# Kernel tuning notes

Measured on AMD Instinct MI355X. Metric: run time of the kernel, lower is better.

The kernel has to match this reference:

```python
import jax, jax.numpy as jnp
import numpy as np

N, F_IN, H, C, E = 100000, 512, 16, 40, 3200000
EPS = 1e-5


def setup_inputs() -> dict:
    key = jax.random.key(0)
    ks = jax.random.split(key, 8)
    x = jax.random.normal(ks[0], (N, F_IN), dtype=jnp.float32)
    edge_index = jax.random.randint(ks[1], (2, E), 0, N, dtype=jnp.int64)
    s1 = 1.0 / np.sqrt(F_IN)
    s2 = 1.0 / np.sqrt(H)
    W1 = jax.random.uniform(ks[2], (F_IN, H), jnp.float32, -s1, s1)
    b1 = jnp.zeros((H,), jnp.float32)
    W2 = jax.random.uniform(ks[3], (H, C), jnp.float32, -s2, s2)
    b2 = jnp.zeros((C,), jnp.float32)
    gamma = jnp.ones((H,), jnp.float32)
    beta = jnp.zeros((H,), jnp.float32)
    return {"x": x, "edge_index": edge_index, "W1": W1, "b1": b1,
            "W2": W2, "b2": b2, "gamma": gamma, "beta": beta}


def gcn_conv(x, edge_index, W, b):
    # PyG GCNConv: linear transform, add self-loops, symmetric normalization,
    # scatter-add aggregation at target nodes (edge_index[1]).
    xw = x @ W  # [N, out]
    loops = jnp.arange(N, dtype=edge_index.dtype)
    row = jnp.concatenate([edge_index[0], loops])  # sources
    col = jnp.concatenate([edge_index[1], loops])  # targets
    deg = jax.ops.segment_sum(jnp.ones_like(col, dtype=xw.dtype), col, num_segments=N)
    dis = jnp.where(deg > 0, jax.lax.rsqrt(deg), 0.0)
    norm = dis[row] * dis[col]  # [E+N]
    msgs = norm[:, None] * xw[row]
    out = jax.ops.segment_sum(msgs, col, num_segments=N)
    return out + b


def batch_norm(x, gamma, beta):
    mean = jnp.mean(x, axis=0)
    var = jnp.var(x, axis=0)
    return (x - mean) * jax.lax.rsqrt(var + EPS) * gamma + beta


def reference(x, edge_index, W1, b1, W2, b2, gamma, beta):
    h = jax.nn.relu(gcn_conv(x, edge_index, W1, b1))
    h = batch_norm(h, gamma, beta)
    # dropout omitted (deterministic reference / eval)
    h = gcn_conv(h, edge_index, W2, b2)
    return jax.nn.log_softmax(h, axis=1)
```

## Files before the change

kernel.cpp:

```cpp
#include <hip/hip_runtime.h>

#define NN 100000
#define FIN 512
#define HD 16
#define CD 40
#define NE 3200000
#define EPSV 1e-5f
#define NBUK 391
#define CAP 9216
#define CH 4096
#define NBLK_CNT ((NE + CH - 1) / CH)
#define NBLK_MM ((NN / 16 + 3) / 4)
#define NSTAT 256

typedef __attribute__((ext_vector_type(8))) short short8;
typedef __attribute__((ext_vector_type(4))) float f32x4;

static __device__ __forceinline__ short f2bf(float f) {
  union { float f; unsigned u; } a; a.f = f;
  unsigned r = a.u + 0x7fffu + ((a.u >> 16) & 1u);
  return (short)(r >> 16);
}
static __device__ __forceinline__ float bf2f(unsigned short u) {
  union { unsigned u; float f; } a; a.u = (unsigned)u << 16; return a.f;
}

__global__ void k_init(int* __restrict__ bkcur, int* __restrict__ gbase) {
  int i = threadIdx.x;
  if (i < NBUK) bkcur[i] = 0;
  if (i == 0) *gbase = 0;
}

__global__ void __launch_bounds__(256) k_fat(const int* __restrict__ ei,
                                             int* __restrict__ bkcur,
                                             unsigned* __restrict__ part,
                                             const float* __restrict__ x,
                                             const float* __restrict__ W1,
                                             float* __restrict__ xw) {
  __shared__ unsigned stg[CH];
  __shared__ unsigned spk[CH];
  __shared__ int hist[NBUK];
  __shared__ int lbase[NBUK + 1];
  __shared__ int gb[NBUK];
  int t = threadIdx.x;
  if (blockIdx.x % 3 == 0) {
    int pb = blockIdx.x / 3;
    int e0 = pb * CH;
    int n = NE - e0; if (n > CH) n = CH;
    for (int i = t; i < NBUK; i += 256) hist[i] = 0;
    for (int i = t; i < n; i += 256) stg[i] = (unsigned)ei[NE + e0 + i];
    __syncthreads();
    for (int i = t; i < n; i += 256) atomicAdd(&hist[stg[i] >> 8], 1);
    __syncthreads();
    if (t < 64) {
      int c0 = t * 7;
      int loc[7]; int s = 0;
#pragma unroll
      for (int k = 0; k < 7; k++) {
        int idx = c0 + k;
        int v = (idx < NBUK) ? hist[idx] : 0;
        loc[k] = s; s += v;
      }
      int inc = s;
#pragma unroll
      for (int m = 1; m < 64; m <<= 1) {
        int u = __shfl_up(inc, m);
        if (t >= m) inc += u;
      }
      int base0 = inc - s;
#pragma unroll
      for (int k = 0; k < 7; k++) {
        int idx = c0 + k;
        if (idx < NBUK) lbase[idx] = base0 + loc[k];
      }
      if (t == 63) lbase[NBUK] = base0 + s;
    }
    __syncthreads();
    for (int i = t; i < NBUK; i += 256) {
      int c = hist[i];
      gb[i] = (c > 0) ? atomicAdd(&bkcur[i], c) : 0;
    }
    __syncthreads();
    for (int i = t; i < NBUK; i += 256) hist[i] = lbase[i];
    __syncthreads();
    for (int i = t; i < n; i += 256) {
      unsigned tg = stg[i];
      int b = tg >> 8;
      int pos = atomicAdd(&hist[b], 1);
      spk[pos] = (unsigned)ei[e0 + i] | ((tg & 255u) << 20);
    }
    __syncthreads();
    for (int b = t; b < NBUK; b += 256) {
      int s0 = lbase[b], s1 = lbase[b + 1];
      for (int j = s0; j < s1; j++) stg[j] = (unsigned)b;
    }
    __syncthreads();
    for (int i = t; i < n; i += 256) {
      int b = (int)stg[i];
      int slot = gb[b] + (i - lbase[b]);
      if (slot < CAP) part[(size_t)b * CAP + slot] = spk[i];
    }
  } else {
    int mb = blockIdx.x - blockIdx.x / 3 - 1;
    int wave = t >> 6;
    int lane = t & 63;
    int tile = mb * 4 + wave;
    int row0 = tile * 16;
    if (row0 >= NN) return;
    int lr = lane & 15;
    int kg = lane >> 4;

    short8 bfrag[16];
#pragma unroll
    for (int s = 0; s < 16; s++) {
      int kbase = s * 32 + kg * 8;
      short8 bf;
#pragma unroll
      for (int i = 0; i < 8; i++) bf[i] = f2bf(W1[(kbase + i) * HD + lr]);
      bfrag[s] = bf;
    }

    f32x4 acc = {0.f, 0.f, 0.f, 0.f};
    const float* xrow = x + (size_t)(row0 + lr) * FIN + kg * 8;
    f32x4 a0[4], a1[4];
#pragma unroll
    for (int p = 0; p < 3; p++) {
      a0[p] = *(const f32x4*)(xrow + p * 32);
      a1[p] = *(const f32x4*)(xrow + p * 32 + 4);
    }
#pragma unroll
    for (int s = 0; s < 16; s++) {
      if (s < 13) {
        a0[(s + 3) & 3] = *(const f32x4*)(xrow + (s + 3) * 32);
        a1[(s + 3) & 3] = *(const f32x4*)(xrow + (s + 3) * 32 + 4);
      }
      f32x4 u0 = a0[s & 3], u1 = a1[s & 3];
      short8 af;
      af[0] = f2bf(u0.x); af[1] = f2bf(u0.y); af[2] = f2bf(u0.z); af[3] = f2bf(u0.w);
      af[4] = f2bf(u1.x); af[5] = f2bf(u1.y); af[6] = f2bf(u1.z); af[7] = f2bf(u1.w);
      acc = __builtin_amdgcn_mfma_f32_16x16x32_bf16(af, bfrag[s], acc, 0, 0, 0);
    }
#pragma unroll
    for (int i = 0; i < 4; i++)
      xw[(size_t)(row0 + kg * 4 + i) * HD + lr] = acc[i];
  }
}

__global__ void __launch_bounds__(1024) k_bucket(const int* __restrict__ bkcur,
                                                 const unsigned* __restrict__ part,
                                                 const float* __restrict__ xw,
                                                 int* __restrict__ gbase,
                                                 int* __restrict__ off,
                                                 int* __restrict__ offe,
                                                 float* __restrict__ dis,
                                                 unsigned short* __restrict__ y1b,
                                                 int* __restrict__ srcs) {
  __shared__ unsigned ssrc[CAP];
  __shared__ int lh[256];
  __shared__ int lb[256];
  __shared__ int base_s;
  int b = blockIdx.x, t = threadIdx.x;
  int cnt = bkcur[b]; if (cnt > CAP) cnt = CAP;
  const unsigned* bp = part + (size_t)b * CAP;
  if (t < 256) lh[t] = 0;
  __syncthreads();
  for (int i = t; i < cnt; i += 1024) atomicAdd(&lh[(bp[i] >> 20) & 255], 1);
  __syncthreads();
  int h = 0;
  if (t < 256) { h = lh[t]; lb[t] = h; }
  __syncthreads();
  for (int d = 1; d < 256; d <<= 1) {
    int u = (t < 256 && t >= d) ? lb[t - d] : 0;
    __syncthreads();
    if (t < 256) lb[t] += u;
    __syncthreads();
  }
  if (t == 255) base_s = atomicAdd(gbase, lb[255]);
  __syncthreads();
  int base = base_s;
  if (t < 256) {
    int excl = lb[t] - h;
    int node = (b << 8) + t;
    if (node < NN) {
      off[node] = base + excl;
      offe[node] = base + excl + h;
      float d = rsqrtf((float)(1 + h));
      dis[node] = d;
      const f32x4* xp = (const f32x4*)(xw + (size_t)node * HD);
      f32x4 v0 = xp[0] * d, v1 = xp[1] * d, v2 = xp[2] * d, v3 = xp[3] * d;
      short8 r0, r1;
      r0[0] = f2bf(v0.x); r0[1] = f2bf(v0.y); r0[2] = f2bf(v0.z); r0[3] = f2bf(v0.w);
      r0[4] = f2bf(v1.x); r0[5] = f2bf(v1.y); r0[6] = f2bf(v1.z); r0[7] = f2bf(v1.w);
      r1[0] = f2bf(v2.x); r1[1] = f2bf(v2.y); r1[2] = f2bf(v2.z); r1[3] = f2bf(v2.w);
      r1[4] = f2bf(v3.x); r1[5] = f2bf(v3.y); r1[6] = f2bf(v3.z); r1[7] = f2bf(v3.w);
      short8* yp = (short8*)(y1b + (size_t)node * HD);
      yp[0] = r0; yp[1] = r1;
    }
    lh[t] = excl;
  }
  __syncthreads();
  for (int i = t; i < cnt; i += 1024) {
    unsigned p = bp[i];
    int pos = atomicAdd(&lh[(p >> 20) & 255], 1);
    ssrc[pos] = p & 0xFFFFFu;
  }
  __syncthreads();
  for (int i = t; i < cnt; i += 1024) srcs[base + i] = (int)ssrc[i];
}

__global__ void __launch_bounds__(256) k_g1(const int* __restrict__ off,
                                            const int* __restrict__ offe,
                                            const int* __restrict__ srcs,
                                            const float* __restrict__ dis,
                                            const unsigned short* __restrict__ y1b,
                                            const float* __restrict__ b1,
                                            float* __restrict__ h) {
  int node = (blockIdx.x * blockDim.x + threadIdx.x) >> 6;
  if (node >= NN) return;
  int lane = threadIdx.x & 63;
  int c = lane & 15, g = lane >> 4;
  int start = off[node], end = offe[node];
  float acc = 0.f;
  int i = start + g;
  for (; i + 12 < end; i += 16) {
    int r0 = srcs[i];
    int r1 = srcs[i + 4];
    int r2 = srcs[i + 8];
    int r3 = srcs[i + 12];
    acc += (bf2f(y1b[(size_t)r0 * HD + c]) + bf2f(y1b[(size_t)r1 * HD + c])) +
           (bf2f(y1b[(size_t)r2 * HD + c]) + bf2f(y1b[(size_t)r3 * HD + c]));
  }
  for (; i < end; i += 4) acc += bf2f(y1b[(size_t)srcs[i] * HD + c]);
  acc += __shfl_xor(acc, 16);
  acc += __shfl_xor(acc, 32);
  if (g == 0) {
    float d = dis[node];
    float v = d * (bf2f(y1b[(size_t)node * HD + c]) + acc) + b1[c];
    h[(size_t)node * HD + c] = fmaxf(v, 0.f);
  }
}

__global__ void __launch_bounds__(256) k_stats(const float* __restrict__ h,
                                               float* __restrict__ partial) {
  __shared__ float wsum[4][32];
  int stride = gridDim.x * blockDim.x;
  int t0 = blockIdx.x * blockDim.x + threadIdx.x;
  f32x4 s = {0.f, 0.f, 0.f, 0.f}, s2 = {0.f, 0.f, 0.f, 0.f};
  for (int t = t0; t < NN * 4; t += stride) {
    f32x4 v = ((const f32x4*)h)[t];
    s += v; s2 += v * v;
  }
#pragma unroll
  for (int m = 4; m < 64; m <<= 1) {
    s.x += __shfl_xor(s.x, m);  s.y += __shfl_xor(s.y, m);
    s.z += __shfl_xor(s.z, m);  s.w += __shfl_xor(s.w, m);
    s2.x += __shfl_xor(s2.x, m); s2.y += __shfl_xor(s2.y, m);
    s2.z += __shfl_xor(s2.z, m); s2.w += __shfl_xor(s2.w, m);
  }
  int wave = threadIdx.x >> 6, lane = threadIdx.x & 63;
  if (lane < 4) {
    int cb = lane * 4;
    wsum[wave][cb + 0] = s.x;  wsum[wave][cb + 1] = s.y;
    wsum[wave][cb + 2] = s.z;  wsum[wave][cb + 3] = s.w;
    wsum[wave][16 + cb + 0] = s2.x; wsum[wave][16 + cb + 1] = s2.y;
    wsum[wave][16 + cb + 2] = s2.z; wsum[wave][16 + cb + 3] = s2.w;
  }
  __syncthreads();
  if (threadIdx.x < 32) {
    float a = ((wsum[0][threadIdx.x] + wsum[1][threadIdx.x]) +
               (wsum[2][threadIdx.x] + wsum[3][threadIdx.x]));
    partial[blockIdx.x * 32 + threadIdx.x] = a;
  }
}

__global__ void __launch_bounds__(256) k_y2(const float* __restrict__ h,
                                            const float* __restrict__ partial,
                                            const float* __restrict__ gamma,
                                            const float* __restrict__ beta,
                                            const float* __restrict__ dis,
                                            unsigned short* __restrict__ y2b) {
  __shared__ float raw[32];
  __shared__ float scs[16], shs[16];
  int j = threadIdx.x;
  if (j < 32) {
    float a = 0.f;
    for (int b = 0; b < NSTAT; b++) a += partial[b * 32 + j];
    raw[j] = a;
  }
  __syncthreads();
  if (j < 16) {
    float mean = raw[j] * (1.0f / NN);
    float var = raw[16 + j] * (1.0f / NN) - mean * mean;
    float inv = rsqrtf(var + EPSV);
    float sc = gamma[j] * inv;
    scs[j] = sc;
    shs[j] = beta[j] - mean * sc;
  }
  __syncthreads();
  int node = blockIdx.x * blockDim.x + j;
  if (node >= NN) return;
  float d = dis[node];
  const f32x4* hp = (const f32x4*)(h + (size_t)node * HD);
  const f32x4* scp = (const f32x4*)scs;
  const f32x4* shp = (const f32x4*)shs;
  f32x4 v0 = (hp[0] * scp[0] + shp[0]) * d;
  f32x4 v1 = (hp[1] * scp[1] + shp[1]) * d;
  f32x4 v2 = (hp[2] * scp[2] + shp[2]) * d;
  f32x4 v3 = (hp[3] * scp[3] + shp[3]) * d;
  short8 r0, r1;
  r0[0] = f2bf(v0.x); r0[1] = f2bf(v0.y); r0[2] = f2bf(v0.z); r0[3] = f2bf(v0.w);
  r0[4] = f2bf(v1.x); r0[5] = f2bf(v1.y); r0[6] = f2bf(v1.z); r0[7] = f2bf(v1.w);
  r1[0] = f2bf(v2.x); r1[1] = f2bf(v2.y); r1[2] = f2bf(v2.z); r1[3] = f2bf(v2.w);
  r1[4] = f2bf(v3.x); r1[5] = f2bf(v3.y); r1[6] = f2bf(v3.z); r1[7] = f2bf(v3.w);
  short8* yp = (short8*)(y2b + (size_t)node * HD);
  yp[0] = r0; yp[1] = r1;
}

__global__ void __launch_bounds__(256) k_g2(const int* __restrict__ off,
                                            const int* __restrict__ offe,
                                            const int* __restrict__ srcs,
                                            const float* __restrict__ dis,
                                            const unsigned short* __restrict__ y2b,
                                            const float* __restrict__ W2,
                                            const float* __restrict__ b2,
                                            float* __restrict__ out) {
  int node = (blockIdx.x * blockDim.x + threadIdx.x) >> 6;
  if (node >= NN) return;
  int lane = threadIdx.x & 63;
  int c = lane & 15, g = lane >> 4;
  int start = off[node], end = offe[node];
  float acc = 0.f;
  int i = start + g;
  for (; i + 12 < end; i += 16) {
    int r0 = srcs[i];
    int r1 = srcs[i + 4];
    int r2 = srcs[i + 8];
    int r3 = srcs[i + 12];
    acc += (bf2f(y2b[(size_t)r0 * HD + c]) + bf2f(y2b[(size_t)r1 * HD + c])) +
           (bf2f(y2b[(size_t)r2 * HD + c]) + bf2f(y2b[(size_t)r3 * HD + c]));
  }
  for (; i < end; i += 4) acc += bf2f(y2b[(size_t)srcs[i] * HD + c]);
  acc += __shfl_xor(acc, 16);
  acc += __shfl_xor(acc, 32);
  float d = dis[node];
  float r = d * (bf2f(y2b[(size_t)node * HD + c]) + acc);
  int cls = lane;
  float z = (cls < CD) ? b2[cls] : 0.f;
#pragma unroll
  for (int k = 0; k < HD; k++) {
    float rk = __shfl(r, k);
    if (cls < CD) z += rk * W2[k * CD + cls];
  }
  float zz = (cls < CD) ? z : -1e30f;
#pragma unroll
  for (int m = 1; m < 64; m <<= 1) zz = fmaxf(zz, __shfl_xor(zz, m));
  float e = (cls < CD) ? __expf(z - zz) : 0.f;
#pragma unroll
  for (int m = 1; m < 64; m <<= 1) e += __shfl_xor(e, m);
  float l = __logf(e) + zz;
  if (cls < CD) out[(size_t)node * CD + cls] = z - l;
}

extern "C" void kernel_launch(void* const* d_in, const int* in_sizes, int n_in,
                              void* d_out, int out_size, void* d_ws, size_t ws_size,
                              hipStream_t stream) {
  const float* x     = (const float*)d_in[0];
  const int*   ei    = (const int*)d_in[1];
  const float* W1    = (const float*)d_in[2];
  const float* b1    = (const float*)d_in[3];
  const float* W2    = (const float*)d_in[4];
  const float* b2    = (const float*)d_in[5];
  const float* gamma = (const float*)d_in[6];
  const float* beta  = (const float*)d_in[7];
  float* out = (float*)d_out;

  float* ws = (float*)d_ws;
  float*          dis     = ws;
  float*          partial = ws + NN;
  float*          xw      = partial + NSTAT * 32;
  unsigned short* y1b     = (unsigned short*)(xw + (size_t)NN * HD);
  float*          h       = (float*)(y1b + (size_t)NN * HD);
  unsigned short* y2b     = (unsigned short*)(h + (size_t)NN * HD);
  int*            off     = (int*)(y2b + (size_t)NN * HD);
  int*            offe    = off + NN;
  int*            srcs    = offe + NN;
  int*            bkcur   = srcs + NE;
  int*            gbase   = bkcur + NBUK;
  unsigned*       part    = (unsigned*)(gbase + 1);

  const int nblk_n  = (NN + 255) / 256;
  const int nblk_gw = (NN * 64 + 255) / 256;

  k_init<<<1, 512, 0, stream>>>(bkcur, gbase);
  k_fat<<<NBLK_CNT + NBLK_MM, 256, 0, stream>>>(ei, bkcur, part, x, W1, xw);
  k_bucket<<<NBUK, 1024, 0, stream>>>(bkcur, part, xw, gbase, off, offe, dis, y1b, srcs);
  k_g1<<<nblk_gw, 256, 0, stream>>>(off, offe, srcs, dis, y1b, b1, h);
  k_stats<<<NSTAT, 256, 0, stream>>>(h, partial);
  k_y2<<<nblk_n, 256, 0, stream>>>(h, partial, gamma, beta, dis, y2b);
  k_g2<<<nblk_gw, 256, 0, stream>>>(off, offe, srcs, dis, y2b, W2, b2, out);
}
```

Baseline: 233.4 us.

## Stage x tiles into LDS via async global_load_lds with double buffering

The matmul path of the fused kernel now streams x through LDS using direct global-to-LDS async loads, double-buffered in 64-column chunks with a rotated (swizzled) layout. Previously it used register prefetch of strided global loads. The shared memory of both block roles is unioned into one buffer so the matmul waves can reuse it. This aims for coalesced, latency-hidden loads of the large x read, at the cost of LDS traffic, manual vmcnt waits, and higher LDS use per block, which may lower occupancy.

After: 229.8 us. About the same (-1.5%).

```diff
diff --git a/kernel.cpp b/kernel.cpp
--- a/kernel.cpp
+++ b/kernel.cpp
@@ -12,6 +12,7 @@
 #define NBLK_CNT ((NE + CH - 1) / CH)
 #define NBLK_MM ((NN / 16 + 3) / 4)
 #define NSTAT 256
+#define SMEM_BYTES 37504
 
 typedef __attribute__((ext_vector_type(8))) short short8;
 typedef __attribute__((ext_vector_type(4))) float f32x4;
@@ -23,6 +24,11 @@
 }
 static __device__ __forceinline__ float bf2f(unsigned short u) {
   union { unsigned u; float f; } a; a.u = (unsigned)u << 16; return a.f;
+}
+static __device__ __forceinline__ void gload_lds(const float* g, float* l) {
+  __builtin_amdgcn_global_load_lds(
+      (const __attribute__((address_space(1))) void*)g,
+      (__attribute__((address_space(3))) void*)l, 16, 0, 0);
 }
 
 __global__ void k_init(int* __restrict__ bkcur, int* __restrict__ gbase) {
@@ -37,13 +43,14 @@
                                              const float* __restrict__ x,
                                              const float* __restrict__ W1,
                                              float* __restrict__ xw) {
-  __shared__ unsigned stg[CH];
-  __shared__ unsigned spk[CH];
-  __shared__ int hist[NBUK];
-  __shared__ int lbase[NBUK + 1];
-  __shared__ int gb[NBUK];
+  __shared__ __align__(16) char smem_u[SMEM_BYTES];
   int t = threadIdx.x;
   if (blockIdx.x % 3 == 0) {
+    unsigned* stg   = (unsigned*)smem_u;
+    unsigned* spk   = stg + CH;
+    int*      hist  = (int*)(spk + CH);
+    int*      lbase = hist + NBUK;
+    int*      gb    = lbase + NBUK + 1;
     int pb = blockIdx.x / 3;
     int e0 = pb * CH;
     int n = NE - e0; if (n > CH) n = CH;
@@ -109,6 +116,7 @@
     if (row0 >= NN) return;
     int lr = lane & 15;
     int kg = lane >> 4;
+    float* xs = (float*)smem_u + wave * 2048;
 
     short8 bfrag[16];
 #pragma unroll
@@ -120,26 +128,44 @@
       bfrag[s] = bf;
     }
 
+    const float* xbase = x + (size_t)row0 * FIN;
+    int rr = lane >> 4;
+    int pos = lane & 15;
+#define STAGE(c)                                                         \
+    {                                                                    \
+      float* dst = xs + ((c) & 1) * 1024;                                \
+      _Pragma("unroll")                                                  \
+      for (int j = 0; j < 4; j++) {                                      \
+        int row = j * 4 + rr;                                            \
+        int u = (pos - row) & 15;                                        \
+        gload_lds(xbase + (size_t)row * FIN + (c) * 64 + u * 4,          \
+                  dst + j * 256);                                        \
+      }                                                                  \
+    }
+
+    STAGE(0);
+    STAGE(1);
     f32x4 acc = {0.f, 0.f, 0.f, 0.f};
-    const float* xrow = x + (size_t)(row0 + lr) * FIN + kg * 8;
-    f32x4 a0[4], a1[4];
-#pragma unroll
-    for (int p = 0; p < 3; p++) {
-      a0[p] = *(const f32x4*)(xrow + p * 32);
-      a1[p] = *(const f32x4*)(xrow + p * 32 + 4);
-    }
-#pragma unroll
-    for (int s = 0; s < 16; s++) {
-      if (s < 13) {
-        a0[(s + 3) & 3] = *(const f32x4*)(xrow + (s + 3) * 32);
-        a1[(s + 3) & 3] = *(const f32x4*)(xrow + (s + 3) * 32 + 4);
+#pragma unroll
+    for (int c = 0; c < 8; c++) {
+      if (c < 7) { asm volatile("s_waitcnt vmcnt(4)" ::: "memory"); }
+      else       { asm volatile("s_waitcnt vmcnt(0)" ::: "memory"); }
+      __builtin_amdgcn_sched_barrier(0);
+      const float* bufp = xs + (c & 1) * 1024;
+#pragma unroll
+      for (int s2 = 0; s2 < 2; s2++) {
+        int lu0 = s2 * 8 + 2 * kg;
+        f32x4 u0 = *(const f32x4*)(bufp + lr * 64 + ((lu0 + lr) & 15) * 4);
+        f32x4 u1 = *(const f32x4*)(bufp + lr * 64 + ((lu0 + 1 + lr) & 15) * 4);
+        short8 af;
+        af[0] = f2bf(u0.x); af[1] = f2bf(u0.y); af[2] = f2bf(u0.z); af[3] = f2bf(u0.w);
+        af[4] = f2bf(u1.x); af[5] = f2bf(u1.y); af[6] = f2bf(u1.z); af[7] = f2bf(u1.w);
+        acc = __builtin_amdgcn_mfma_f32_16x16x32_bf16(af, bfrag[c * 2 + s2], acc, 0, 0, 0);
       }
-      f32x4 u0 = a0[s & 3], u1 = a1[s & 3];
-      short8 af;
-      af[0] = f2bf(u0.x); af[1] = f2bf(u0.y); af[2] = f2bf(u0.z); af[3] = f2bf(u0.w);
-      af[4] = f2bf(u1.x); af[5] = f2bf(u1.y); af[6] = f2bf(u1.z); af[7] = f2bf(u1.w);
-      acc = __builtin_amdgcn_mfma_f32_16x16x32_bf16(af, bfrag[s], acc, 0, 0, 0);
-    }
+      __builtin_amdgcn_sched_barrier(0);
+      if (c < 6) STAGE(c + 2);
+    }
+#undef STAGE
 #pragma unroll
     for (int i = 0; i < 4; i++)
       xw[(size_t)(row0 + kg * 4 + i) * HD + lr] = acc[i];
@@ -388,11 +414,12 @@
   int*            gbase   = bkcur + NBUK;
   unsigned*       part    = (unsigned*)(gbase + 1);
 
-  const int nblk_n  = (NN + 255) / 256;
-  const int nblk_gw = (NN * 64 + 255) / 256;
+  const int nblk_n   = (NN + 255) / 256;
+  const int nblk_gw  = (NN * 64 + 255) / 256;
+  const int nblk_fat = NBLK_CNT + NBLK_MM;
 
   k_init<<<1, 512, 0, stream>>>(bkcur, gbase);
-  k_fat<<<NBLK_CNT + NBLK_MM, 256, 0, stream>>>(ei, bkcur, part, x, W1, xw);
+  k_fat<<<nblk_fat, 256, 0, stream>>>(ei, bkcur, part, x, W1, xw);
   k_bucket<<<NBUK, 1024, 0, stream>>>(bkcur, part, xw, gbase, off, offe, dis, y1b, srcs);
   k_g1<<<nblk_gw, 256, 0, stream>>>(off, offe, srcs, dis, y1b, b1, h);
   k_stats<<<NSTAT, 256, 0, stream>>>(h, partial);
```

## Split fused GEMM into bf16 conversion pass plus separate MFMA kernel

Applied to the files above, without the earlier changes.

The fused kernel's matmul blocks now only convert x from fp32 to bf16 and write it to a workspace buffer. A new separate kernel then runs the MFMA projection reading the bf16 copy with deeper prefetch. This adds a full extra write and read of a 100MB-scale buffer (bf16 x) and an extra launch. The likely goal is a simpler, more latency-tolerant GEMM kernel, but the extra traffic is substantial.

Result: slower. 271.4 us (+16.3%).

```diff
diff --git a/kernel.cpp b/kernel.cpp
--- a/kernel.cpp
+++ b/kernel.cpp
@@ -12,6 +12,7 @@
 #define NBLK_CNT ((NE + CH - 1) / CH)
 #define NBLK_MM ((NN / 16 + 3) / 4)
 #define NSTAT 256
+#define NELEM ((size_t)NN * FIN)
 
 typedef __attribute__((ext_vector_type(8))) short short8;
 typedef __attribute__((ext_vector_type(4))) float f32x4;
@@ -31,12 +32,11 @@
   if (i == 0) *gbase = 0;
 }
 
-__global__ void __launch_bounds__(256) k_fat(const int* __restrict__ ei,
-                                             int* __restrict__ bkcur,
-                                             unsigned* __restrict__ part,
-                                             const float* __restrict__ x,
-                                             const float* __restrict__ W1,
-                                             float* __restrict__ xw) {
+__global__ void __launch_bounds__(256) k_fat1(const int* __restrict__ ei,
+                                              int* __restrict__ bkcur,
+                                              unsigned* __restrict__ part,
+                                              const float* __restrict__ x,
+                                              unsigned short* __restrict__ xb) {
   __shared__ unsigned stg[CH];
   __shared__ unsigned spk[CH];
   __shared__ int hist[NBUK];
@@ -101,49 +101,56 @@
       if (slot < CAP) part[(size_t)b * CAP + slot] = spk[i];
     }
   } else {
-    int mb = blockIdx.x - blockIdx.x / 3 - 1;
-    int wave = t >> 6;
-    int lane = t & 63;
-    int tile = mb * 4 + wave;
-    int row0 = tile * 16;
-    if (row0 >= NN) return;
-    int lr = lane & 15;
-    int kg = lane >> 4;
-
-    short8 bfrag[16];
-#pragma unroll
-    for (int s = 0; s < 16; s++) {
-      int kbase = s * 32 + kg * 8;
-      short8 bf;
-#pragma unroll
-      for (int i = 0; i < 8; i++) bf[i] = f2bf(W1[(kbase + i) * HD + lr]);
-      bfrag[s] = bf;
-    }
-
-    f32x4 acc = {0.f, 0.f, 0.f, 0.f};
-    const float* xrow = x + (size_t)(row0 + lr) * FIN + kg * 8;
-    f32x4 a0[4], a1[4];
-#pragma unroll
-    for (int p = 0; p < 3; p++) {
-      a0[p] = *(const f32x4*)(xrow + p * 32);
-      a1[p] = *(const f32x4*)(xrow + p * 32 + 4);
-    }
-#pragma unroll
-    for (int s = 0; s < 16; s++) {
-      if (s < 13) {
-        a0[(s + 3) & 3] = *(const f32x4*)(xrow + (s + 3) * 32);
-        a1[(s + 3) & 3] = *(const f32x4*)(xrow + (s + 3) * 32 + 4);
+    int cb = blockIdx.x - blockIdx.x / 3 - 1;
+    size_t base = (size_t)cb * 32768;
+#pragma unroll 4
+    for (int it = 0; it < 16; it++) {
+      size_t idx = base + (size_t)it * 2048 + t * 8;
+      if (idx < NELEM) {
+        f32x4 v0 = *(const f32x4*)(x + idx);
+        f32x4 v1 = *(const f32x4*)(x + idx + 4);
+        short8 r;
+        r[0] = f2bf(v0.x); r[1] = f2bf(v0.y); r[2] = f2bf(v0.z); r[3] = f2bf(v0.w);
+        r[4] = f2bf(v1.x); r[5] = f2bf(v1.y); r[6] = f2bf(v1.z); r[7] = f2bf(v1.w);
+        *(short8*)(xb + idx) = r;
       }
-      f32x4 u0 = a0[s & 3], u1 = a1[s & 3];
-      short8 af;
-      af[0] = f2bf(u0.x); af[1] = f2bf(u0.y); af[2] = f2bf(u0.z); af[3] = f2bf(u0.w);
-      af[4] = f2bf(u1.x); af[5] = f2bf(u1.y); af[6] = f2bf(u1.z); af[7] = f2bf(u1.w);
-      acc = __builtin_amdgcn_mfma_f32_16x16x32_bf16(af, bfrag[s], acc, 0, 0, 0);
-    }
-#pragma unroll
-    for (int i = 0; i < 4; i++)
-      xw[(size_t)(row0 + kg * 4 + i) * HD + lr] = acc[i];
-  }
+    }
+  }
+}
+
+__global__ void __launch_bounds__(256) k_mm(const unsigned short* __restrict__ xb,
+                                            const float* __restrict__ W1,
+                                            float* __restrict__ xw) {
+  int t = threadIdx.x;
+  int wave = t >> 6, lane = t & 63;
+  int tile = blockIdx.x * 4 + wave;
+  int row0 = tile * 16;
+  if (row0 >= NN) return;
+  int lr = lane & 15, kg = lane >> 4;
+
+  short8 bfrag[16];
+#pragma unroll
+  for (int s = 0; s < 16; s++) {
+    int kbase = s * 32 + kg * 8;
+    short8 bf;
+#pragma unroll
+    for (int i = 0; i < 8; i++) bf[i] = f2bf(W1[(kbase + i) * HD + lr]);
+    bfrag[s] = bf;
+  }
+
+  const unsigned short* xrow = xb + (size_t)(row0 + lr) * FIN + kg * 8;
+  short8 a[8];
+#pragma unroll
+  for (int p = 0; p < 7; p++) a[p] = *(const short8*)(xrow + p * 32);
+  f32x4 acc = {0.f, 0.f, 0.f, 0.f};
+#pragma unroll
+  for (int s = 0; s < 16; s++) {
+    if (s < 9) a[(s + 7) & 7] = *(const short8*)(xrow + (s + 7) * 32);
+    acc = __builtin_amdgcn_mfma_f32_16x16x32_bf16(a[s & 7], bfrag[s], acc, 0, 0, 0);
+  }
+#pragma unroll
+  for (int i = 0; i < 4; i++)
+    xw[(size_t)(row0 + kg * 4 + i) * HD + lr] = acc[i];
 }
 
 __global__ void __launch_bounds__(1024) k_bucket(const int* __restrict__ bkcur,
@@ -387,12 +394,15 @@
   int*            bkcur   = srcs + NE;
   int*            gbase   = bkcur + NBUK;
   unsigned*       part    = (unsigned*)(gbase + 1);
-
-  const int nblk_n  = (NN + 255) / 256;
-  const int nblk_gw = (NN * 64 + 255) / 256;
+  unsigned short* xb      = (unsigned short*)(part + (size_t)NBUK * CAP);
+
+  const int nblk_n   = (NN + 255) / 256;
+  const int nblk_gw  = (NN * 64 + 255) / 256;
+  const int nblk_fat = NBLK_CNT + NBLK_MM;
 
   k_init<<<1, 512, 0, stream>>>(bkcur, gbase);
-  k_fat<<<NBLK_CNT + NBLK_MM, 256, 0, stream>>>(ei, bkcur, part, x, W1, xw);
+  k_fat1<<<nblk_fat, 256, 0, stream>>>(ei, bkcur, part, x, xb);
+  k_mm<<<NBLK_MM, 256, 0, stream>>>(xb, W1, xw);
   k_bucket<<<NBUK, 1024, 0, stream>>>(bkcur, part, xw, gbase, off, offe, dis, y1b, srcs);
   k_g1<<<nblk_gw, 256, 0, stream>>>(off, offe, srcs, dis, y1b, b1, h);
   k_stats<<<NSTAT, 256, 0, stream>>>(h, partial);
```
